# Performance work log

Measured on AMD Instinct MI355X. Metric: run time of the kernel, lower is better.

Reference implementation:

```python
import jax, jax.numpy as jnp
from jax import lax
import numpy as np

TAG_NAMES = ["O", "B-MAT", "I-MAT", "B-PRO", "I-PRO", "B-APL", "I-APL", "B-SMT", "I-SMT", "B-CMT", "I-CMT", "B-DSC", "I-DSC"]
IMP = -100.0


def _init_crf_params(key):
    # torchcrf initializes uniform(-0.1, 0.1); CRF_NEW then clamps invalid
    # BIO transitions to -100 per define_invalid_crf_transitions/init_crf_transitions.
    K = len(TAG_NAMES)
    k1, k2, k3 = jax.random.split(key, 3)
    start = np.array(jax.random.uniform(k1, (K,), minval=-0.1, maxval=0.1), dtype=np.float32)
    end = np.array(jax.random.uniform(k2, (K,), minval=-0.1, maxval=0.1), dtype=np.float32)
    trans = np.array(jax.random.uniform(k3, (K, K), minval=-0.1, maxval=0.1), dtype=np.float32)
    pref = [t[0] for t in TAG_NAMES]
    ent = [t.split('-')[1] if '-' in t else '' for t in TAG_NAMES]
    for i in range(K):
        if pref[i] in ('B', 'I'):  # invalid begin/end for BIO
            start[i] = IMP
            end[i] = IMP
    for i in range(K):
        for j in range(K):
            # invalid_transitions_position: O -> I  (B->P, I->P are empty sets)
            if pref[i] == 'O' and pref[j] == 'I':
                trans[i, j] = IMP
            # invalid_transitions_tags: B->I, I->I across different entity types
            if pref[i] in ('B', 'I') and pref[j] == 'I' and ent[i] != ent[j]:
                trans[i, j] = IMP
    return jnp.asarray(start), jnp.asarray(end), jnp.asarray(trans)


def setup_inputs() -> dict:
    key = jax.random.key(0)
    k_em, k_tag, k_p = jax.random.split(key, 3)
    B, T, K = 4096, 512, len(TAG_NAMES)
    emissions = jax.random.normal(k_em, (B, T, K), dtype=jnp.float32)
    tags = jax.random.randint(k_tag, (B, T), 0, K, dtype=jnp.int64)
    mask = jnp.ones((B, T), dtype=bool)
    start_transitions, end_transitions, transitions = _init_crf_params(k_p)
    return {"emissions": emissions, "tags": tags, "mask": mask,
            "start_transitions": start_transitions,
            "end_transitions": end_transitions,
            "transitions": transitions}


def reference(emissions, tags, mask, start_transitions, end_transitions, transitions):
    # torchcrf CRF.forward with batch_first=True, reduction='sum':
    # returns sum over batch of log p(tags | emissions).
    B, T, K = emissions.shape
    maskf = mask.astype(emissions.dtype)

    # ---- numerator: score of the given tag path ----
    emit = jnp.take_along_axis(emissions, tags[..., None], axis=2)[..., 0]  # [B,T]
    trans = transitions[tags[:, :-1], tags[:, 1:]]                           # [B,T-1]
    num = start_transitions[tags[:, 0]] + emit[:, 0]
    num = num + jnp.sum((trans + emit[:, 1:]) * maskf[:, 1:], axis=1)
    seq_ends = jnp.sum(mask.astype(jnp.int32), axis=1) - 1                   # [B]
    last_tags = tags[jnp.arange(B), seq_ends]
    num = num + end_transitions[last_tags]

    # ---- denominator: log partition via forward-algorithm scan over time ----
    em_t = jnp.swapaxes(emissions, 0, 1)   # [T,B,K]
    mask_t = jnp.swapaxes(mask, 0, 1)      # [T,B]
    score0 = start_transitions + em_t[0]   # [B,K]

    def step(score, xs):
        em, m = xs  # em: [B,K], m: [B]
        # broadcast: [B,K_from,1] + [K_from,K_to] + [B,1,K_to]
        nxt = jax.nn.logsumexp(score[:, :, None] + transitions[None] + em[:, None, :], axis=1)
        return jnp.where(m[:, None], nxt, score), None

    score, _ = lax.scan(step, score0, (em_t[1:], mask_t[1:]))
    denom = jax.nn.logsumexp(score + end_transitions, axis=1)  # [B]

    return jnp.sum(num - denom)
```

## Files before the change

### kernel.cpp

```cpp
#include <hip/hip_runtime.h>


#define ROR(n) (0x120 + (n))

template<int C>
__device__ __forceinline__ int dpp_i(int x) {
  return __builtin_amdgcn_update_dpp(x, x, C, 0xF, 0xF, false);
}
template<int C>
__device__ __forceinline__ float dpp_f(float x) {
  return __int_as_float(dpp_i<C>(__float_as_int(x)));
}

__global__ void __launch_bounds__(128, 2)
crf_main(const float* __restrict__ em,
         const int*   __restrict__ tags,
         const float* __restrict__ startT,
         const float* __restrict__ endT,
         const float* __restrict__ trans,
         float* __restrict__ partial)
{
  constexpr int T = 512, K = 13;
  __shared__ float ldsT[K * K];
  __shared__ float pF[4][16];
  __shared__ float metaF[4][2];
  __shared__ float blk[4];
  const int tid = threadIdx.x;
  for (int i = tid; i < K * K; i += 128) ldsT[i] = trans[i];
  __syncthreads();

  const int lane = tid & 63;
  const int j    = lane & 15;
  const int jc   = (j < K) ? j : (K - 1);
  const int row  = lane >> 4;
  const int b    = blockIdx.x * 4 + row;
  const size_t bOff = (size_t)b * T * K;
  const size_t tOff = (size_t)b * T;
  const bool is_fwd = (tid < 64);

  int src[16];
  src[0]  = j;
  src[1]  = dpp_i<ROR(1)>(j);   src[2]  = dpp_i<ROR(2)>(j);
  src[3]  = dpp_i<ROR(3)>(j);   src[4]  = dpp_i<ROR(4)>(j);
  src[5]  = dpp_i<ROR(5)>(j);   src[6]  = dpp_i<ROR(6)>(j);
  src[7]  = dpp_i<ROR(7)>(j);   src[8]  = dpp_i<ROR(8)>(j);
  src[9]  = dpp_i<ROR(9)>(j);   src[10] = dpp_i<ROR(10)>(j);
  src[11] = dpp_i<ROR(11)>(j);  src[12] = dpp_i<ROR(12)>(j);
  src[13] = dpp_i<ROR(13)>(j);  src[14] = dpp_i<ROR(14)>(j);
  src[15] = dpp_i<ROR(15)>(j);

  float C16[16];
#pragma unroll
  for (int r = 0; r < 16; ++r) {
    const int si = src[r];
    C16[r] = (si < K && j < K)
           ? __expf(is_fwd ? ldsT[si * K + j] : ldsT[j * K + si])
           : 0.0f;
  }

  float p = 0.0f, logscale = 0.0f, em_acc = 0.0f, trans_acc = 0.0f;
  int tg_last = 0;
  float em_b[16]; int tg_b[16]; float tv_b[8];

#define TREE(q) do {                                                   \
    float a0 = (q) * C16[0];                                           \
    float a1 = dpp_f<ROR(1)>(q) * C16[1];                              \
    float a2 = dpp_f<ROR(2)>(q) * C16[2];                              \
    float a3 = dpp_f<ROR(3)>(q) * C16[3];                              \
    a0 = fmaf(dpp_f<ROR(4)>(q),  C16[4],  a0);                         \
    a1 = fmaf(dpp_f<ROR(5)>(q),  C16[5],  a1);                         \
    a2 = fmaf(dpp_f<ROR(6)>(q),  C16[6],  a2);                         \
    a3 = fmaf(dpp_f<ROR(7)>(q),  C16[7],  a3);                         \
    a0 = fmaf(dpp_f<ROR(8)>(q),  C16[8],  a0);                         \
    a1 = fmaf(dpp_f<ROR(9)>(q),  C16[9],  a1);                         \
    a2 = fmaf(dpp_f<ROR(10)>(q), C16[10], a2);                         \
    a3 = fmaf(dpp_f<ROR(11)>(q), C16[11], a3);                         \
    a0 = fmaf(dpp_f<ROR(12)>(q), C16[12], a0);                         \
    a1 = fmaf(dpp_f<ROR(13)>(q), C16[13], a1);                         \
    a2 = fmaf(dpp_f<ROR(14)>(q), C16[14], a2);                         \
    a3 = fmaf(dpp_f<ROR(15)>(q), C16[15], a3);                         \
    tree = (a0 + a1) + (a2 + a3);                                      \
  } while (0)

#define RENORM() do {                                                  \
    float m_ = p;                                                      \
    m_ = fmaxf(m_, dpp_f<ROR(1)>(m_));                                 \
    m_ = fmaxf(m_, dpp_f<ROR(2)>(m_));                                 \
    m_ = fmaxf(m_, dpp_f<ROR(4)>(m_));                                 \
    m_ = fmaxf(m_, dpp_f<ROR(8)>(m_));                                 \
    p *= __builtin_amdgcn_rcpf(m_);                                    \
    logscale += __logf(m_);                                            \
  } while (0)

#define STEPF(s, RN) do {                                              \
    const float emt = em_b[s];                                         \
    const int   tg  = tg_b[s];                                         \
    const float eem = __expf(emt);                                     \
    float tree;                                                        \
    TREE(p);                                                           \
    p = tree * eem;                                                    \
    em_acc   += (tg == j) ? emt : 0.0f;                                \
    trans_acc += tv_b[(s) & 7];                                        \
    if (RN) RENORM();                                                  \
  } while (0)

#define STEPB(s, RN) do {                                              \
    const float emt = em_b[s];                                         \
    const int   tg  = tg_b[s];                                         \
    const float eem = __expf(emt);                                     \
    const float y   = p * eem;                                         \
    float tree;                                                        \
    TREE(y);                                                           \
    p = tree;                                                          \
    em_acc   += (tg == j) ? emt : 0.0f;                                \
    trans_acc += tv_b[(s) & 7];                                        \
    if (RN) RENORM();                                                  \
  } while (0)

#define TVPF(k, A, B) \
    tv_b[(k) & 7] = ldsT[tg_b[(A) & 15] * K + tg_b[(B) & 15]]

  if (is_fwd) {
    const float em0 = em[bOff + jc];
    const int   tg0 = tags[tOff];
    p = (j < K) ? __expf(startT[j] + em0) : 0.0f;
    const float start_t0 = startT[tg0];
    em_acc = (tg0 == j) ? em0 : 0.0f;

    const float* emc = em + bOff + jc + K;
    const int*   tgc = tags + tOff + 1;
#pragma unroll
    for (int r = 0; r < 16; ++r) { em_b[r] = emc[r * K]; tg_b[r] = tgc[r]; }
#pragma unroll
    for (int r = 0; r < 8; ++r) {
      const int a = (r == 0) ? tg0 : tg_b[r - 1];
      tv_b[r] = ldsT[a * K + tg_b[r]];
    }

    for (int c = 0; c < 15; ++c) {
#pragma unroll
      for (int k = 0; k < 16; ++k) {
        STEPF(k, (k == 7 || k == 15));
        TVPF(k, k + 7, k + 8);
        em_b[k] = emc[(k + 16) * K];
        tg_b[k] = tgc[k + 16];
      }
      emc += 16 * K; tgc += 16;
    }
#pragma unroll
    for (int k = 0; k < 15; ++k) {
      STEPF(k, (k == 7));
      if (k < 7) TVPF(k, k + 7, k + 8);
    }

    float ems = em_acc;
    ems += dpp_f<ROR(1)>(ems);
    ems += dpp_f<ROR(2)>(ems);
    ems += dpp_f<ROR(4)>(ems);
    ems += dpp_f<ROR(8)>(ems);
    pF[row][j] = p;
    if (j == 0) {
      metaF[row][0] = logscale;
      metaF[row][1] = start_t0 + ems + trans_acc;
    }
  } else {
    p = (j < K) ? __expf(endT[j]) : 0.0f;

    const float* emc = em + bOff + jc + (size_t)(T - 1) * K;
    const int*   tgc = tags + tOff + (T - 1);
#pragma unroll
    for (int r = 0; r < 16; ++r) { em_b[r] = emc[-r * K]; tg_b[r] = tgc[-r]; }
    tg_last = tg_b[0];
#pragma unroll
    for (int r = 0; r < 8; ++r)
      tv_b[r] = ldsT[tg_b[r + 1] * K + tg_b[r]];

    for (int c = 0; c < 15; ++c) {
#pragma unroll
      for (int k = 0; k < 16; ++k) {
        STEPB(k, (k == 7 || k == 15));
        TVPF(k, k + 9, k + 8);
        em_b[k] = emc[-(k + 16) * K];
        tg_b[k] = tgc[-(k + 16)];
      }
      emc -= 16 * K; tgc -= 16;
    }
#pragma unroll
    for (int k = 0; k < 16; ++k) {
      STEPB(k, (k == 7));
      if (k < 7) TVPF(k, k + 9, k + 8);
    }
  }

  __syncthreads();

  if (!is_fwd) {
    float ems = em_acc;
    ems += dpp_f<ROR(1)>(ems);
    ems += dpp_f<ROR(2)>(ems);
    ems += dpp_f<ROR(4)>(ems);
    ems += dpp_f<ROR(8)>(ems);
    float v = p * pF[row][j];
    v += dpp_f<ROR(1)>(v);
    v += dpp_f<ROR(2)>(v);
    v += dpp_f<ROR(4)>(v);
    v += dpp_f<ROR(8)>(v);
    const float denom = metaF[row][0] + logscale + __logf(v);
    const float num   = metaF[row][1] + ems + trans_acc + endT[tg_last];
    if (j == 0) blk[row] = num - denom;
  }
  __syncthreads();
  if (tid == 0) partial[blockIdx.x] = (blk[0] + blk[1]) + (blk[2] + blk[3]);

#undef TREE
#undef RENORM
#undef STEPF
#undef STEPB
#undef TVPF
}

__global__ void __launch_bounds__(256)
crf_reduce(const float* __restrict__ part, float* __restrict__ out, int n)
{
  float v = 0.0f;
  for (int i = threadIdx.x; i < n; i += 256) v += part[i];
#pragma unroll
  for (int off = 32; off > 0; off >>= 1) v += __shfl_down(v, off);
  __shared__ float w[4];
  if ((threadIdx.x & 63) == 0) w[threadIdx.x >> 6] = v;
  __syncthreads();
  if (threadIdx.x == 0) out[0] = (w[0] + w[1]) + (w[2] + w[3]);
}

extern "C" void kernel_launch(void* const* d_in, const int* in_sizes, int n_in,
                              void* d_out, int out_size, void* d_ws, size_t ws_size,
                              hipStream_t stream) {
  const float* em   = (const float*)d_in[0];
  const int*   tags = (const int*)d_in[1];
  const float* st   = (const float*)d_in[3];
  const float* en   = (const float*)d_in[4];
  const float* tr   = (const float*)d_in[5];
  float* part = (float*)d_ws;

  crf_main<<<1024, 128, 0, stream>>>(em, tags, st, en, tr, part);
  crf_reduce<<<1, 256, 0, stream>>>(part, (float*)d_out, 1024);
}
```

Before: 195.9 us.

## Double-buffer emission/tag loads in 16-step chunks with vectorized tag reads

Replaces the per-step rolling prefetch with a ping-pong double buffer of 16 emissions and 16 tags, loading the next chunk before the current chunk is computed, with sched_barrier fences keeping the two phases apart. Tags are read as int4 vectors, and the transition lookups for a chunk are issued together before its steps run. The transition table in LDS is padded to a row stride of 16 so indexing uses shifts. The goal is to hide global load latency behind the serial recurrence and to cut per-step load instructions, in exchange for more registers and duplicated barriers in the divergent forward/backward branches.

```diff
diff --git a/kernel.cpp b/kernel.cpp
--- a/kernel.cpp
+++ b/kernel.cpp
@@ -11,6 +11,15 @@
 __device__ __forceinline__ float dpp_f(float x) {
   return __int_as_float(dpp_i<C>(__float_as_int(x)));
 }
+
+__device__ __forceinline__ int tg_at(const int4* tb, int k) {
+  const int4 v = tb[k >> 2];
+  const int m = k & 3;
+  return m == 0 ? v.x : m == 1 ? v.y : m == 2 ? v.z : v.w;
+}
+
+#define FENCE do { __builtin_amdgcn_sched_barrier(0); \
+                   asm volatile("" ::: "memory"); } while (0)
 
 __global__ void __launch_bounds__(128, 2)
 crf_main(const float* __restrict__ em,
@@ -20,13 +29,16 @@
          const float* __restrict__ trans,
          float* __restrict__ partial)
 {
-  constexpr int T = 512, K = 13;
-  __shared__ float ldsT[K * K];
+  constexpr int T = 512, K = 13, KP = 16;
+  __shared__ float ldsT[13 * KP];
   __shared__ float pF[4][16];
   __shared__ float metaF[4][2];
   __shared__ float blk[4];
   const int tid = threadIdx.x;
-  for (int i = tid; i < K * K; i += 128) ldsT[i] = trans[i];
+  for (int i = tid; i < 169; i += 128) {
+    const int r_ = i / 13, c_ = i - r_ * 13;
+    ldsT[r_ * KP + c_] = trans[i];
+  }
   __syncthreads();
 
   const int lane = tid & 63;
@@ -54,13 +66,14 @@
   for (int r = 0; r < 16; ++r) {
     const int si = src[r];
     C16[r] = (si < K && j < K)
-           ? __expf(is_fwd ? ldsT[si * K + j] : ldsT[j * K + si])
+           ? __expf(is_fwd ? ldsT[si * KP + j] : ldsT[j * KP + si])
            : 0.0f;
   }
 
   float p = 0.0f, logscale = 0.0f, em_acc = 0.0f, trans_acc = 0.0f;
-  int tg_last = 0;
-  float em_b[16]; int tg_b[16]; float tv_b[8];
+  float emA[16], emB[16], tv[16];
+  int4  tgA[4], tgB[4];
+  int   tg_prev = 0;
 
 #define TREE(q) do {                                                   \
     float a0 = (q) * C16[0];                                           \
@@ -92,66 +105,103 @@
     logscale += __logf(m_);                                            \
   } while (0)
 
-#define STEPF(s, RN) do {                                              \
-    const float emt = em_b[s];                                         \
-    const int   tg  = tg_b[s];                                         \
-    const float eem = __expf(emt);                                     \
-    float tree;                                                        \
-    TREE(p);                                                           \
-    p = tree * eem;                                                    \
-    em_acc   += (tg == j) ? emt : 0.0f;                                \
-    trans_acc += tv_b[(s) & 7];                                        \
-    if (RN) RENORM();                                                  \
-  } while (0)
-
-#define STEPB(s, RN) do {                                              \
-    const float emt = em_b[s];                                         \
-    const int   tg  = tg_b[s];                                         \
-    const float eem = __expf(emt);                                     \
-    const float y   = p * eem;                                         \
-    float tree;                                                        \
-    TREE(y);                                                           \
-    p = tree;                                                          \
-    em_acc   += (tg == j) ? emt : 0.0f;                                \
-    trans_acc += tv_b[(s) & 7];                                        \
-    if (RN) RENORM();                                                  \
-  } while (0)
-
-#define TVPF(k, A, B) \
-    tv_b[(k) & 7] = ldsT[tg_b[(A) & 15] * K + tg_b[(B) & 15]]
+#define LOADF(EB, TB) do {                                             \
+    _Pragma("unroll")                                                  \
+    for (int k_ = 0; k_ < 16; ++k_) EB[k_] = emcL[k_ * K];             \
+    const int4* tp_ = (const int4*)tgcL;                               \
+    TB[0] = tp_[0]; TB[1] = tp_[1]; TB[2] = tp_[2]; TB[3] = tp_[3];    \
+    emcL += 16 * K; tgcL += 16;                                        \
+  } while (0)
+
+#define LOADB(EB, TB) do {                                             \
+    _Pragma("unroll")                                                  \
+    for (int k_ = 0; k_ < 16; ++k_) EB[k_] = emcL[-(k_ * K)];          \
+    const int4* tp_ = (const int4*)tgcL;                               \
+    TB[0] = tp_[0]; TB[1] = tp_[1]; TB[2] = tp_[2]; TB[3] = tp_[3];    \
+    emcL -= 16 * K; tgcL -= 16;                                        \
+  } while (0)
+
+#define TVISS_F(TB, K0) do {                                           \
+    int a_ = tg_prev;                                                  \
+    _Pragma("unroll")                                                  \
+    for (int k_ = K0; k_ < 16; ++k_) {                                 \
+      const int b_ = tg_at(TB, k_);                                    \
+      tv[k_] = ldsT[a_ * KP + b_];                                     \
+      a_ = b_;                                                         \
+    }                                                                  \
+    tg_prev = a_;                                                      \
+  } while (0)
+
+#define TVISS_B(TB) do {                                               \
+    int a_ = tg_prev;                                                  \
+    _Pragma("unroll")                                                  \
+    for (int k_ = 0; k_ < 16; ++k_) {                                  \
+      const int b_ = tg_at(TB, 15 - k_);                               \
+      tv[k_] = ldsT[b_ * KP + a_];                                     \
+      a_ = b_;                                                         \
+    }                                                                  \
+    tg_prev = a_;                                                      \
+  } while (0)
+
+#define STEPSF(EB, TB, K0) do {                                        \
+    _Pragma("unroll")                                                  \
+    for (int k_ = K0; k_ < 16; ++k_) {                                 \
+      const float emt = EB[k_];                                        \
+      const int   tg  = tg_at(TB, k_);                                 \
+      const float eem = __expf(emt);                                   \
+      float tree; TREE(p);                                             \
+      p = tree * eem;                                                  \
+      em_acc   += (tg == j) ? emt : 0.0f;                              \
+      trans_acc += tv[k_];                                             \
+      if (k_ == 7 || k_ == 15) RENORM();                               \
+    }                                                                  \
+  } while (0)
+
+#define STEPSB(EB, TB) do {                                            \
+    _Pragma("unroll")                                                  \
+    for (int k_ = 0; k_ < 16; ++k_) {                                  \
+      const float emt = EB[k_];                                        \
+      const int   tg  = tg_at(TB, 15 - k_);                            \
+      const float eem = __expf(emt);                                   \
+      const float y   = p * eem;                                       \
+      float tree; TREE(y);                                             \
+      p = tree;                                                        \
+      em_acc   += (tg == j) ? emt : 0.0f;                              \
+      trans_acc += tv[k_];                                             \
+      if (k_ == 7 || k_ == 15) RENORM();                               \
+    }                                                                  \
+  } while (0)
 
   if (is_fwd) {
-    const float em0 = em[bOff + jc];
-    const int   tg0 = tags[tOff];
+    const float* emcL = em + bOff + jc;
+    const int*   tgcL = tags + tOff;
+    const float em0 = emcL[0];
+#pragma unroll
+    for (int k = 1; k < 16; ++k) emA[k] = emcL[k * K];
+    { const int4* tp = (const int4*)tgcL;
+      tgA[0] = tp[0]; tgA[1] = tp[1]; tgA[2] = tp[2]; tgA[3] = tp[3]; }
+    const int t256 = tgcL[256];
+    emcL += 16 * K; tgcL += 16;
+    LOADF(emB, tgB);
+    FENCE;
+
     p = (j < K) ? __expf(startT[j] + em0) : 0.0f;
+    const int   tg0      = tg_at(tgA, 0);
     const float start_t0 = startT[tg0];
-    em_acc = (tg0 == j) ? em0 : 0.0f;
-
-    const float* emc = em + bOff + jc + K;
-    const int*   tgc = tags + tOff + 1;
-#pragma unroll
-    for (int r = 0; r < 16; ++r) { em_b[r] = emc[r * K]; tg_b[r] = tgc[r]; }
-#pragma unroll
-    for (int r = 0; r < 8; ++r) {
-      const int a = (r == 0) ? tg0 : tg_b[r - 1];
-      tv_b[r] = ldsT[a * K + tg_b[r]];
+    em_acc  = (tg0 == j) ? em0 : 0.0f;
+    tg_prev = tg0;
+
+    TVISS_F(tgA, 1);
+    STEPSF(emA, tgA, 1);
+    for (int it = 0; it < 7; ++it) {
+      LOADF(emA, tgA); FENCE;
+      TVISS_F(tgB, 0); STEPSF(emB, tgB, 0);
+      LOADF(emB, tgB); FENCE;
+      TVISS_F(tgA, 0); STEPSF(emA, tgA, 0);
     }
-
-    for (int c = 0; c < 15; ++c) {
-#pragma unroll
-      for (int k = 0; k < 16; ++k) {
-        STEPF(k, (k == 7 || k == 15));
-        TVPF(k, k + 7, k + 8);
-        em_b[k] = emc[(k + 16) * K];
-        tg_b[k] = tgc[k + 16];
-      }
-      emc += 16 * K; tgc += 16;
-    }
-#pragma unroll
-    for (int k = 0; k < 15; ++k) {
-      STEPF(k, (k == 7));
-      if (k < 7) TVPF(k, k + 7, k + 8);
-    }
+    FENCE;
+    TVISS_F(tgB, 0); STEPSF(emB, tgB, 0);
+    trans_acc += ldsT[tg_prev * KP + t256];
 
     float ems = em_acc;
     ems += dpp_f<ROR(1)>(ems);
@@ -163,38 +213,36 @@
       metaF[row][0] = logscale;
       metaF[row][1] = start_t0 + ems + trans_acc;
     }
+    __syncthreads();
+    __syncthreads();
   } else {
+    const float* emcL = em + bOff + jc + (size_t)511 * K;
+    const int*   tgcL = tags + tOff + 496;
+#pragma unroll
+    for (int k = 0; k < 16; ++k) emA[k] = emcL[-(k * K)];
+    { const int4* tp = (const int4*)tgcL;
+      tgA[0] = tp[0]; tgA[1] = tp[1]; tgA[2] = tp[2]; tgA[3] = tp[3]; }
+    emcL -= 16 * K; tgcL -= 16;
+    LOADB(emB, tgB);
+    FENCE;
+
     p = (j < K) ? __expf(endT[j]) : 0.0f;
-
-    const float* emc = em + bOff + jc + (size_t)(T - 1) * K;
-    const int*   tgc = tags + tOff + (T - 1);
-#pragma unroll
-    for (int r = 0; r < 16; ++r) { em_b[r] = emc[-r * K]; tg_b[r] = tgc[-r]; }
-    tg_last = tg_b[0];
-#pragma unroll
-    for (int r = 0; r < 8; ++r)
-      tv_b[r] = ldsT[tg_b[r + 1] * K + tg_b[r]];
-
-    for (int c = 0; c < 15; ++c) {
-#pragma unroll
-      for (int k = 0; k < 16; ++k) {
-        STEPB(k, (k == 7 || k == 15));
-        TVPF(k, k + 9, k + 8);
-        em_b[k] = emc[-(k + 16) * K];
-        tg_b[k] = tgc[-(k + 16)];
-      }
-      emc -= 16 * K; tgc -= 16;
+    const int tg_last = tg_at(tgA, 15);
+    tg_prev = 0;
+
+    TVISS_B(tgA);
+    tv[0] = 0.0f;
+    STEPSB(emA, tgA);
+    for (int it = 0; it < 7; ++it) {
+      LOADB(emA, tgA); FENCE;
+      TVISS_B(tgB); STEPSB(emB, tgB);
+      LOADB(emB, tgB); FENCE;
+      TVISS_B(tgA); STEPSB(emA, tgA);
     }
-#pragma unroll
-    for (int k = 0; k < 16; ++k) {
-      STEPB(k, (k == 7));
-      if (k < 7) TVPF(k, k + 9, k + 8);
-    }
-  }
-
-  __syncthreads();
-
-  if (!is_fwd) {
+    FENCE;
+    TVISS_B(tgB); STEPSB(emB, tgB);
+
+    __syncthreads();
     float ems = em_acc;
     ems += dpp_f<ROR(1)>(ems);
     ems += dpp_f<ROR(2)>(ems);
@@ -208,15 +256,18 @@
     const float denom = metaF[row][0] + logscale + __logf(v);
     const float num   = metaF[row][1] + ems + trans_acc + endT[tg_last];
     if (j == 0) blk[row] = num - denom;
+    __syncthreads();
   }
-  __syncthreads();
   if (tid == 0) partial[blockIdx.x] = (blk[0] + blk[1]) + (blk[2] + blk[3]);
 
 #undef TREE
 #undef RENORM
-#undef STEPF
-#undef STEPB
-#undef TVPF
+#undef LOADF
+#undef LOADB
+#undef TVISS_F
+#undef TVISS_B
+#undef STEPSF
+#undef STEPSB
 }
 
 __global__ void __launch_bounds__(256)
```

New measurement: 200.5 us. 1.02x slower.

## Stage emission/tag chunks into LDS via async global_load_lds double buffering

Applied to the files above, without the earlier changes.

Each wave stops loading per-lane strided emissions and tags straight into registers. It now issues coalesced global_load_lds DMA copies of 16-timestep chunks for its four sequences into a double-buffered LDS area, and waits on vmcnt before consuming each chunk. The forward and backward recurrences then read emissions and tags from LDS. Transition-score gathers for the numerator are batched once per chunk instead of being prefetched per step. This targets the uncoalesced strided global loads and their register-pipeline cost, at the price of LDS traffic and hand-written waitcnt synchronisation, which is fragile.

```diff
diff --git a/kernel.cpp b/kernel.cpp
--- a/kernel.cpp
+++ b/kernel.cpp
@@ -2,6 +2,9 @@
 
 
 #define ROR(n) (0x120 + (n))
+#define AS1 __attribute__((address_space(1)))
+#define AS3 __attribute__((address_space(3)))
+typedef unsigned int u32;
 
 template<int C>
 __device__ __forceinline__ int dpp_i(int x) {
@@ -11,6 +14,18 @@
 __device__ __forceinline__ float dpp_f(float x) {
   return __int_as_float(dpp_i<C>(__float_as_int(x)));
 }
+__device__ __forceinline__ int tg_at(const int4* tb, int k) {
+  const int4 v = tb[k >> 2];
+  const int m = k & 3;
+  return m == 0 ? v.x : m == 1 ? v.y : m == 2 ? v.z : v.w;
+}
+__device__ __forceinline__ void dma4(const float* g, float* l) {
+  __builtin_amdgcn_global_load_lds((const AS1 u32*)g, (AS3 u32*)l, 4, 0, 0);
+}
+
+#define WAITV14 asm volatile("s_waitcnt vmcnt(14)" ::: "memory")
+#define WAITV0  asm volatile("s_waitcnt vmcnt(0)"  ::: "memory")
+#define WAITL0  asm volatile("s_waitcnt lgkmcnt(0)" ::: "memory")
 
 __global__ void __launch_bounds__(128, 2)
 crf_main(const float* __restrict__ em,
@@ -20,23 +35,42 @@
          const float* __restrict__ trans,
          float* __restrict__ partial)
 {
-  constexpr int T = 512, K = 13;
-  __shared__ float ldsT[K * K];
+  constexpr int K = 13, KP = 16;
+  __shared__ float ws[2][2][896];
+  __shared__ float ldsT[13 * KP];
+  __shared__ float ldsS[16];
+  __shared__ float ldsE[16];
   __shared__ float pF[4][16];
   __shared__ float metaF[4][2];
+  __shared__ int   tag255s[4];
   __shared__ float blk[4];
+
   const int tid = threadIdx.x;
-  for (int i = tid; i < K * K; i += 128) ldsT[i] = trans[i];
+  for (int i = tid; i < 169; i += 128) {
+    const int r_ = i / 13, c_ = i - r_ * 13;
+    ldsT[r_ * KP + c_] = trans[i];
+  }
+  if (tid < 13) ldsS[tid] = startT[tid];
+  else if (tid >= 16 && tid < 29) ldsE[tid - 16] = endT[tid - 16];
   __syncthreads();
 
   const int lane = tid & 63;
   const int j    = lane & 15;
   const int jc   = (j < K) ? j : (K - 1);
   const int row  = lane >> 4;
-  const int b    = blockIdx.x * 4 + row;
-  const size_t bOff = (size_t)b * T * K;
-  const size_t tOff = (size_t)b * T;
-  const bool is_fwd = (tid < 64);
+  const int w    = tid >> 6;
+  const bool is_fwd = (w == 0);
+  const float* emG = em   + (size_t)(blockIdx.x * 4) * 6656;
+  const int*   tgG = tags + (size_t)(blockIdx.x * 4) * 512;
+
+  int srcOff[13];
+#pragma unroll
+  for (int i = 0; i < 13; ++i) {
+    const int e  = i * 64 + lane;
+    const int r_ = e / 208;
+    srcOff[i] = r_ * 6656 + (e - r_ * 208);
+  }
+  const int tagOff = (lane >> 4) * 512 + (lane & 15);
 
   int src[16];
   src[0]  = j;
@@ -48,19 +82,23 @@
   src[11] = dpp_i<ROR(11)>(j);  src[12] = dpp_i<ROR(12)>(j);
   src[13] = dpp_i<ROR(13)>(j);  src[14] = dpp_i<ROR(14)>(j);
   src[15] = dpp_i<ROR(15)>(j);
-
   float C16[16];
 #pragma unroll
   for (int r = 0; r < 16; ++r) {
     const int si = src[r];
     C16[r] = (si < K && j < K)
-           ? __expf(is_fwd ? ldsT[si * K + j] : ldsT[j * K + si])
+           ? __expf(is_fwd ? ldsT[si * KP + j] : ldsT[j * KP + si])
            : 0.0f;
   }
 
-  float p = 0.0f, logscale = 0.0f, em_acc = 0.0f, trans_acc = 0.0f;
-  int tg_last = 0;
-  float em_b[16]; int tg_b[16]; float tv_b[8];
+#define ISSUE(EMBASE, TBASE, RB) do {                                  \
+    float* rb_ = (RB);                                                 \
+    const int eb_ = (EMBASE);                                          \
+    _Pragma("unroll")                                                  \
+    for (int i_ = 0; i_ < 13; ++i_)                                    \
+      dma4(emG + eb_ + srcOff[i_], rb_ + i_ * 64);                     \
+    dma4((const float*)(tgG + (TBASE) + tagOff), rb_ + 832);           \
+  } while (0)
 
 #define TREE(q) do {                                                   \
     float a0 = (q) * C16[0];                                           \
@@ -92,67 +130,47 @@
     logscale += __logf(m_);                                            \
   } while (0)
 
-#define STEPF(s, RN) do {                                              \
-    const float emt = em_b[s];                                         \
-    const int   tg  = tg_b[s];                                         \
-    const float eem = __expf(emt);                                     \
-    float tree;                                                        \
-    TREE(p);                                                           \
-    p = tree * eem;                                                    \
-    em_acc   += (tg == j) ? emt : 0.0f;                                \
-    trans_acc += tv_b[(s) & 7];                                        \
-    if (RN) RENORM();                                                  \
-  } while (0)
-
-#define STEPB(s, RN) do {                                              \
-    const float emt = em_b[s];                                         \
-    const int   tg  = tg_b[s];                                         \
-    const float eem = __expf(emt);                                     \
-    const float y   = p * eem;                                         \
-    float tree;                                                        \
-    TREE(y);                                                           \
-    p = tree;                                                          \
-    em_acc   += (tg == j) ? emt : 0.0f;                                \
-    trans_acc += tv_b[(s) & 7];                                        \
-    if (RN) RENORM();                                                  \
-  } while (0)
-
-#define TVPF(k, A, B) \
-    tv_b[(k) & 7] = ldsT[tg_b[(A) & 15] * K + tg_b[(B) & 15]]
+  float p = 0.0f, logscale = 0.0f, em_acc = 0.0f, trans_acc = 0.0f;
+  const int emBase = row * 208 + jc;
 
   if (is_fwd) {
-    const float em0 = em[bOff + jc];
-    const int   tg0 = tags[tOff];
-    p = (j < K) ? __expf(startT[j] + em0) : 0.0f;
-    const float start_t0 = startT[tg0];
-    em_acc = (tg0 == j) ? em0 : 0.0f;
-
-    const float* emc = em + bOff + jc + K;
-    const int*   tgc = tags + tOff + 1;
-#pragma unroll
-    for (int r = 0; r < 16; ++r) { em_b[r] = emc[r * K]; tg_b[r] = tgc[r]; }
-#pragma unroll
-    for (int r = 0; r < 8; ++r) {
-      const int a = (r == 0) ? tg0 : tg_b[r - 1];
-      tv_b[r] = ldsT[a * K + tg_b[r]];
+    ISSUE(0, 0, ws[w][0]);
+    ISSUE(208, 16, ws[w][1]);
+    float start_t0 = 0.0f;
+    int tg_hi = 0;
+    for (int c = 0; c < 16; ++c) {
+      if (c == 15) { WAITV0; } else { WAITV14; }
+      float* rb = ws[w][c & 1];
+      const float* rbE = rb;
+      int4 tq[4];
+      { const int4* tp = (const int4*)((const int*)(rb + 832) + (row << 4));
+        tq[0] = tp[0]; tq[1] = tp[1]; tq[2] = tp[2]; tq[3] = tp[3]; }
+      float tsum = 0.0f;
+#pragma unroll
+      for (int k = 0; k < 15; ++k)
+        tsum += ldsT[tg_at(tq, k) * KP + tg_at(tq, k + 1)];
+      if (c) tsum += ldsT[tg_hi * KP + tg_at(tq, 0)];
+      tg_hi = tg_at(tq, 15);
+      trans_acc += tsum;
+#pragma unroll
+      for (int k = 0; k < 16; ++k) {
+        const float emt = rbE[emBase + k * 13];
+        const int   tg  = tg_at(tq, k);
+        if (k == 0 && c == 0) {
+          p = (j < K) ? __expf(ldsS[j] + emt) : 0.0f;
+          em_acc = (tg == j) ? emt : 0.0f;
+          start_t0 = ldsS[tg];
+        } else {
+          const float eem = __expf(emt);
+          float tree; TREE(p);
+          p = tree * eem;
+          em_acc += (tg == j) ? emt : 0.0f;
+        }
+        if (k == 7 || k == 15) RENORM();
+      }
+      WAITL0;
+      if (c < 14) ISSUE(208 * (c + 2), 16 * (c + 2), ws[w][c & 1]);
     }
-
-    for (int c = 0; c < 15; ++c) {
-#pragma unroll
-      for (int k = 0; k < 16; ++k) {
-        STEPF(k, (k == 7 || k == 15));
-        TVPF(k, k + 7, k + 8);
-        em_b[k] = emc[(k + 16) * K];
-        tg_b[k] = tgc[k + 16];
-      }
-      emc += 16 * K; tgc += 16;
-    }
-#pragma unroll
-    for (int k = 0; k < 15; ++k) {
-      STEPF(k, (k == 7));
-      if (k < 7) TVPF(k, k + 7, k + 8);
-    }
-
     float ems = em_acc;
     ems += dpp_f<ROR(1)>(ems);
     ems += dpp_f<ROR(2)>(ems);
@@ -162,39 +180,46 @@
     if (j == 0) {
       metaF[row][0] = logscale;
       metaF[row][1] = start_t0 + ems + trans_acc;
+      tag255s[row]  = tg_hi;
     }
+    __syncthreads();
+    __syncthreads();
   } else {
-    p = (j < K) ? __expf(endT[j]) : 0.0f;
-
-    const float* emc = em + bOff + jc + (size_t)(T - 1) * K;
-    const int*   tgc = tags + tOff + (T - 1);
-#pragma unroll
-    for (int r = 0; r < 16; ++r) { em_b[r] = emc[-r * K]; tg_b[r] = tgc[-r]; }
-    tg_last = tg_b[0];
-#pragma unroll
-    for (int r = 0; r < 8; ++r)
-      tv_b[r] = ldsT[tg_b[r + 1] * K + tg_b[r]];
-
-    for (int c = 0; c < 15; ++c) {
-#pragma unroll
-      for (int k = 0; k < 16; ++k) {
-        STEPB(k, (k == 7 || k == 15));
-        TVPF(k, k + 9, k + 8);
-        em_b[k] = emc[-(k + 16) * K];
-        tg_b[k] = tgc[-(k + 16)];
+    ISSUE(6448, 496, ws[w][0]);
+    ISSUE(6240, 480, ws[w][1]);
+    p = (j < K) ? __expf(ldsE[j]) : 0.0f;
+    int tg_lo = 0, tg_last = 0;
+    for (int c = 0; c < 16; ++c) {
+      if (c == 15) { WAITV0; } else { WAITV14; }
+      float* rb = ws[w][c & 1];
+      const float* rbE = rb;
+      int4 tq[4];
+      { const int4* tp = (const int4*)((const int*)(rb + 832) + (row << 4));
+        tq[0] = tp[0]; tq[1] = tp[1]; tq[2] = tp[2]; tq[3] = tp[3]; }
+      float tsum = 0.0f;
+#pragma unroll
+      for (int k = 0; k < 15; ++k)
+        tsum += ldsT[tg_at(tq, k) * KP + tg_at(tq, k + 1)];
+      if (c) tsum += ldsT[tg_at(tq, 15) * KP + tg_lo];
+      else   tg_last = tg_at(tq, 15);
+      tg_lo = tg_at(tq, 0);
+      trans_acc += tsum;
+#pragma unroll
+      for (int kk = 0; kk < 16; ++kk) {
+        const int k = 15 - kk;
+        const float emt = rbE[emBase + k * 13];
+        const int   tg  = tg_at(tq, k);
+        const float eem = __expf(emt);
+        const float y   = p * eem;
+        float tree; TREE(y);
+        p = tree;
+        em_acc += (tg == j) ? emt : 0.0f;
+        if (kk == 7 || kk == 15) RENORM();
       }
-      emc -= 16 * K; tgc -= 16;
+      WAITL0;
+      if (c < 14) ISSUE(6448 - 208 * (c + 2), 496 - 16 * (c + 2), ws[w][c & 1]);
     }
-#pragma unroll
-    for (int k = 0; k < 16; ++k) {
-      STEPB(k, (k == 7));
-      if (k < 7) TVPF(k, k + 9, k + 8);
-    }
-  }
-
-  __syncthreads();
-
-  if (!is_fwd) {
+    __syncthreads();
     float ems = em_acc;
     ems += dpp_f<ROR(1)>(ems);
     ems += dpp_f<ROR(2)>(ems);
@@ -206,17 +231,17 @@
     v += dpp_f<ROR(4)>(v);
     v += dpp_f<ROR(8)>(v);
     const float denom = metaF[row][0] + logscale + __logf(v);
-    const float num   = metaF[row][1] + ems + trans_acc + endT[tg_last];
+    const float num   = metaF[row][1] + ems + trans_acc
+                      + ldsT[tag255s[row] * KP + tg_lo]
+                      + endT[tg_last];
     if (j == 0) blk[row] = num - denom;
-  }
-  __syncthreads();
+    __syncthreads();
+  }
   if (tid == 0) partial[blockIdx.x] = (blk[0] + blk[1]) + (blk[2] + blk[3]);
 
+#undef ISSUE
 #undef TREE
 #undef RENORM
-#undef STEPF
-#undef STEPB
-#undef TVPF
 }
 
 __global__ void __launch_bounds__(256)
@@ -226,10 +251,10 @@
   for (int i = threadIdx.x; i < n; i += 256) v += part[i];
 #pragma unroll
   for (int off = 32; off > 0; off >>= 1) v += __shfl_down(v, off);
-  __shared__ float w[4];
-  if ((threadIdx.x & 63) == 0) w[threadIdx.x >> 6] = v;
+  __shared__ float wsum[4];
+  if ((threadIdx.x & 63) == 0) wsum[threadIdx.x >> 6] = v;
   __syncthreads();
-  if (threadIdx.x == 0) out[0] = (w[0] + w[1]) + (w[2] + w[3]);
+  if (threadIdx.x == 0) out[0] = (wsum[0] + wsum[1]) + (wsum[2] + wsum[3]);
 }
 
 extern "C" void kernel_launch(void* const* d_in, const int* in_sizes, int n_in,
```

Result: slower. 206.7 us (+5.5%).
